# Performance work log

Measured on AMD Instinct MI355X. Metric: run time of the kernel, lower is better.

## Reference

```python
import jax, jax.numpy as jnp
import numpy as np

EPS = 1e-5

def rmsnorm(x):
    # BitLinear pre-norm (no learnable scale), per BitNet b1.58 reference impl
    return x * jax.lax.rsqrt(jnp.mean(x * x, axis=-1, keepdims=True) + EPS)

def act_quant(x):
    # per-token absmax 8-bit quantization with straight-through estimator
    scale = 127.0 / jnp.clip(jnp.max(jnp.abs(x), axis=-1, keepdims=True), 1e-5)
    q = jnp.clip(jnp.round(x * scale), -128.0, 127.0) / scale
    return x + jax.lax.stop_gradient(q - x)

def weight_quant(w):
    # absmean ternary quantization {-1,0,1} with STE
    scale = 1.0 / jnp.clip(jnp.mean(jnp.abs(w)), 1e-5)
    q = jnp.clip(jnp.round(w * scale), -1.0, 1.0) / scale
    return w + jax.lax.stop_gradient(q - w)

def bitlinear(x, w, b):
    # x: [b, s, d_in], w: [d_out, d_in] (torch Linear layout), b: [d_out]
    xq = act_quant(rmsnorm(x))
    wq = weight_quant(w)
    return jnp.einsum('bsd,fd->bsf', xq, wq) + b

def setup_inputs() -> dict:
    key = jax.random.key(0)
    k0, k1, k2 = jax.random.split(key, 3)
    B, S, D, F = 2, 8192, 1024, 4096  # inner_dim = dim * mult = 4096
    x = jax.random.normal(k0, (B, S, D), dtype=jnp.float32)
    w1 = jax.random.normal(k1, (F, D), dtype=jnp.float32) * (1.0 / np.sqrt(D))
    b1 = jnp.zeros((F,), dtype=jnp.float32)
    w2 = jax.random.normal(k2, (D, F), dtype=jnp.float32) * (1.0 / np.sqrt(F))
    b2 = jnp.zeros((D,), dtype=jnp.float32)
    return {"x": x, "w1": w1, "b1": b1, "w2": w2, "b2": b2}

def reference(x, w1, b1, w2, b2):
    h = bitlinear(x, w1, b1)
    h = jax.nn.gelu(h, approximate=False)  # nn.GELU() default is exact
    # post_act_ln=False -> no LayerNorm; dropout p=0.0 -> identity
    return bitlinear(h, w2, b2)
```

## Files before the change

### kernel.cpp

```cpp
#include <hip/hip_runtime.h>
#include <hip/hip_bf16.h>
#include <stdint.h>

typedef int i32x4 __attribute__((ext_vector_type(4)));

__device__ __forceinline__ float blo(unsigned int u) {
  unsigned int v = u << 16; float f; __builtin_memcpy(&f, &v, 4); return f;
}
__device__ __forceinline__ float bhi(unsigned int u) {
  unsigned int v = u & 0xffff0000u; float f; __builtin_memcpy(&f, &v, 4); return f;
}
__device__ __forceinline__ int pack4q(float a, float b, float c, float d, float qm) {
  int i0 = (int)rintf(a * qm) & 255;
  int i1 = (int)rintf(b * qm) & 255;
  int i2 = (int)rintf(c * qm) & 255;
  int i3 = (int)rintf(d * qm) & 255;
  return i0 | (i1 << 8) | (i2 << 16) | (i3 << 24);
}

__device__ __forceinline__ float fast_gelu(float v) {
  float u = v * 0.70710678118654752f;
  float s = fabsf(u);
  float den = fmaf(0.3275911f, s, 1.0f);
  float t;
  asm("v_rcp_f32 %0, %1" : "=v"(t) : "v"(den));
  float p = t * fmaf(t, fmaf(t, fmaf(t, fmaf(t, 1.061405429f, -1.453152027f),
                                     1.421413741f), -0.284496736f), 0.254829592f);
  float e = fmaf(-p, __expf(-u * u), 1.0f);
  float er = copysignf(e, u);
  return 0.5f * v * (1.0f + er);
}

__global__ void k_reduce_abs2(const float* __restrict__ w1, const float* __restrict__ w2,
                              long n4, float* __restrict__ partials) {
  const int half = gridDim.x >> 1;
  const float* w = (blockIdx.x < half) ? w1 : w2;
  int b = (blockIdx.x < half) ? blockIdx.x : blockIdx.x - half;
  const float4* wv = (const float4*)w;
  float s = 0.0f;
  long stride = (long)half * blockDim.x;
  for (long i = (long)b * blockDim.x + threadIdx.x; i < n4; i += stride) {
    float4 v = wv[i];
    s += fabsf(v.x) + fabsf(v.y) + fabsf(v.z) + fabsf(v.w);
  }
  #pragma unroll
  for (int off = 32; off; off >>= 1) s += __shfl_down(s, off);
  __shared__ float sw[4];
  if ((threadIdx.x & 63) == 0) sw[threadIdx.x >> 6] = s;
  __syncthreads();
  if (threadIdx.x == 0) partials[blockIdx.x] = sw[0] + sw[1] + sw[2] + sw[3];
}

__global__ void k_finalize_scales(const float* __restrict__ p1, const float* __restrict__ p2,
                                  float* __restrict__ scales, float inv1, float inv2) {
  int t = threadIdx.x;
  float s1 = p1[t], s2 = p2[t];
  #pragma unroll
  for (int off = 32; off; off >>= 1) { s1 += __shfl_down(s1, off); s2 += __shfl_down(s2, off); }
  __shared__ float a1[4], a2[4];
  if ((t & 63) == 0) { a1[t >> 6] = s1; a2[t >> 6] = s2; }
  __syncthreads();
  if (t == 0) {
    scales[0] = fmaxf((a1[0]+a1[1]+a1[2]+a1[3]) * inv1, 1e-5f);
    scales[1] = fmaxf((a2[0]+a2[1]+a2[2]+a2[3]) * inv2, 1e-5f);
  }
}

__global__ void k_quant_w2(const float* __restrict__ w1, char* __restrict__ wq1,
                           const float* __restrict__ w2, char* __restrict__ wq2,
                           long n4, const float* __restrict__ scales) {
  const int half = gridDim.x >> 1;
  const bool first = blockIdx.x < half;
  const float* w = first ? w1 : w2;
  char* wq = first ? wq1 : wq2;
  int b = first ? blockIdx.x : blockIdx.x - half;
  float s = 1.0f / scales[first ? 0 : 1];
  const float4* wv = (const float4*)w;
  int* qv = (int*)wq;
  long stride = (long)half * blockDim.x;
  for (long i = (long)b * blockDim.x + threadIdx.x; i < n4; i += stride) {
    float4 v = wv[i];
    int b0 = (int)fminf(fmaxf(rintf(v.x * s), -1.0f), 1.0f) & 255;
    int b1 = (int)fminf(fmaxf(rintf(v.y * s), -1.0f), 1.0f) & 255;
    int b2 = (int)fminf(fmaxf(rintf(v.z * s), -1.0f), 1.0f) & 255;
    int b3 = (int)fminf(fmaxf(rintf(v.w * s), -1.0f), 1.0f) & 255;
    qv[i] = b0 | (b1 << 8) | (b2 << 16) | (b3 << 24);
  }
}

__global__ void k_actq_x(const float* __restrict__ x, char* __restrict__ xq,
                         float* __restrict__ alpha) {
  const int D = 1024;
  size_t t = blockIdx.x;
  int tid = threadIdx.x;
  const float4* row = (const float4*)(x + t * (size_t)D);
  float4 v = row[tid];
  float ss = v.x*v.x + v.y*v.y + v.z*v.z + v.w*v.w;
  float am = fmaxf(fmaxf(fabsf(v.x), fabsf(v.y)), fmaxf(fabsf(v.z), fabsf(v.w)));
  #pragma unroll
  for (int off = 32; off; off >>= 1) {
    ss += __shfl_down(ss, off);
    am = fmaxf(am, __shfl_down(am, off));
  }
  __shared__ float s_ss[4], s_am[4];
  if ((tid & 63) == 0) { s_ss[tid >> 6] = ss; s_am[tid >> 6] = am; }
  __syncthreads();
  ss = s_ss[0] + s_ss[1] + s_ss[2] + s_ss[3];
  am = fmaxf(fmaxf(s_am[0], s_am[1]), fmaxf(s_am[2], s_am[3]));
  float rms = rsqrtf(ss * (1.0f / D) + 1e-5f);
  float a   = fmaxf(am * rms, 1e-5f);
  float qs  = 127.0f / a;
  if (tid == 0) alpha[t] = a * (1.0f / 127.0f);
  int b0 = (int)fminf(fmaxf(rintf((v.x * rms) * qs), -128.0f), 127.0f) & 255;
  int b1 = (int)fminf(fmaxf(rintf((v.y * rms) * qs), -128.0f), 127.0f) & 255;
  int b2 = (int)fminf(fmaxf(rintf((v.z * rms) * qs), -128.0f), 127.0f) & 255;
  int b3 = (int)fminf(fmaxf(rintf((v.w * rms) * qs), -128.0f), 127.0f) & 255;
  ((int*)xq)[t * 256 + tid] = b0 | (b1 << 8) | (b2 << 16) | (b3 << 24);
}

__global__ void k_actq_h(__hip_bfloat16* __restrict__ h, float* __restrict__ alpha) {
  const int F = 4096;
  size_t t = blockIdx.x;
  int tid = threadIdx.x;
  char* rb = (char*)(h + t * (size_t)F);
  const uint4* row = (const uint4*)rb;
  uint4 u0 = row[tid], u1 = row[tid + 256];
  unsigned int uu[8] = {u0.x, u0.y, u0.z, u0.w, u1.x, u1.y, u1.z, u1.w};
  float ss = 0.0f, am = 0.0f;
  #pragma unroll
  for (int i = 0; i < 8; i++) {
    float f0 = blo(uu[i]), f1 = bhi(uu[i]);
    ss += f0 * f0 + f1 * f1;
    am = fmaxf(am, fmaxf(fabsf(f0), fabsf(f1)));
  }
  #pragma unroll
  for (int off = 32; off; off >>= 1) {
    ss += __shfl_down(ss, off);
    am = fmaxf(am, __shfl_down(am, off));
  }
  __shared__ float s_ss[4], s_am[4];
  if ((tid & 63) == 0) { s_ss[tid >> 6] = ss; s_am[tid >> 6] = am; }
  __syncthreads();
  ss = s_ss[0] + s_ss[1] + s_ss[2] + s_ss[3];
  am = fmaxf(fmaxf(s_am[0], s_am[1]), fmaxf(s_am[2], s_am[3]));
  float rms = rsqrtf(ss * (1.0f / F) + 1e-5f);
  float a   = fmaxf(am * rms, 1e-5f);
  float qm  = rms * (127.0f / a);
  if (tid == 0) alpha[t] = a * (1.0f / 127.0f);
  uint2 w0, w1;
  w0.x = (unsigned)pack4q(blo(uu[0]), bhi(uu[0]), blo(uu[1]), bhi(uu[1]), qm);
  w0.y = (unsigned)pack4q(blo(uu[2]), bhi(uu[2]), blo(uu[3]), bhi(uu[3]), qm);
  w1.x = (unsigned)pack4q(blo(uu[4]), bhi(uu[4]), blo(uu[5]), bhi(uu[5]), qm);
  w1.y = (unsigned)pack4q(blo(uu[6]), bhi(uu[6]), blo(uu[7]), bhi(uu[7]), qm);
  *(uint2*)(rb + 8 * tid) = w0;
  *(uint2*)(rb + 2048 + 8 * tid) = w1;
}

#define GLD16(GP, LP) __builtin_amdgcn_global_load_lds( \
    (__attribute__((address_space(1))) void*)(GP), \
    (__attribute__((address_space(3))) void*)(LP), 16, 0, 0)
#define VMCNT3 asm volatile("s_waitcnt vmcnt(3)" ::: "memory")
#define VMCNT0 asm volatile("s_waitcnt vmcnt(0)" ::: "memory")
#define LGKM0  do { asm volatile("s_waitcnt lgkmcnt(0)" ::: "memory"); __builtin_amdgcn_sched_barrier(0); } while(0)

template<int EPI>
__global__ __launch_bounds__(512, 4) void k_gemm_i8(
    const char* __restrict__ A, int lda,
    const char* __restrict__ B,
    const float* __restrict__ bias, const float* __restrict__ alpha,
    const float* __restrict__ scales, int which,
    void* __restrict__ Cout, int N, int K, int lgnbx)
{
  __shared__ __align__(16) char lA[3 * 8192];
  __shared__ __align__(16) char lB[3 * 16384];
  const int tid = threadIdx.x, lane = tid & 63, wid = tid >> 6;
  const int wm = wid >> 2, wn = wid & 3;
  const int nwg = gridDim.x, bid = blockIdx.x;
  const int swz = (bid & 7) * (nwg >> 3) + (bid >> 3);
  const int bx = swz & ((1 << lgnbx) - 1), by = swz >> lgnbx;
  const int m0 = by * 128, n0 = bx * 256;
  const int NT = K >> 6;

  const int srow = tid >> 2, slot = tid & 3;
  const int sswz = (slot ^ ((srow >> 1) & 3)) * 16;
  const char* gA0 = A + (size_t)(m0 +       srow) * lda + sswz;
  const char* gB0 = B + (size_t)(n0 +       srow) * K   + sswz;
  const char* gB1 = B + (size_t)(n0 + 128 + srow) * K   + sswz;
  const int ldst = srow * 64 + slot * 16;

  const int lr = lane & 15;
  const int kx = ((lane >> 4) ^ ((lane >> 1) & 3)) * 16;
  const int aoff = (wm * 64 + lr) * 64 + kx;
  const int boff = (wn * 64 + lr) * 64 + kx;

  GLD16(gA0,      lA + ldst);
  GLD16(gB0,      lB + ldst);
  GLD16(gB1,      lB + 8192 + ldst);
  GLD16(gA0 + 64, lA + 8192 + ldst);
  GLD16(gB0 + 64, lB + 16384 + ldst);
  GLD16(gB1 + 64, lB + 16384 + 8192 + ldst);

  i32x4 acc[4][4] = {};
  int cur = 0, nx1 = 1, nx2 = 2;
  for (int t = 0; t < NT; ++t) {
    if (t + 1 < NT) { VMCNT3; } else { VMCNT0; }
    __builtin_amdgcn_s_barrier();
    if (t + 2 < NT) {
      GLD16(gA0 + 64 * (t + 2), lA + nx2 * 8192 + ldst);
      GLD16(gB0 + 64 * (t + 2), lB + nx2 * 16384 + ldst);
      GLD16(gB1 + 64 * (t + 2), lB + nx2 * 16384 + 8192 + ldst);
    }
    i32x4 av[4], bv[4];
    {
      const char* pa = lA + cur * 8192 + aoff;
      const char* pb = lB + cur * 16384 + boff;
      #pragma unroll
      for (int j = 0; j < 4; ++j) av[j] = *(const i32x4*)(pa + j * 1024);
      #pragma unroll
      for (int n = 0; n < 4; ++n) bv[n] = *(const i32x4*)(pb + n * 1024);
    }
    LGKM0;
    __builtin_amdgcn_s_setprio(1);
    #pragma unroll
    for (int j = 0; j < 4; ++j)
      #pragma unroll
      for (int n = 0; n < 4; ++n)
        acc[j][n] = __builtin_amdgcn_mfma_i32_16x16x64_i8(av[j], bv[n], acc[j][n], 0, 0, 0);
    __builtin_amdgcn_s_setprio(0);
    int tmp = cur; cur = nx1; nx1 = nx2; nx2 = tmp;
  }

  const float wdq = scales[which];
  const int lq4 = (lane >> 4) * 4;
  #pragma unroll
  for (int m = 0; m < 4; ++m) {
    const int rowb = m0 + wm * 64 + m * 16 + lq4;
    float al[4];
    #pragma unroll
    for (int q = 0; q < 4; ++q) al[q] = alpha[rowb + q] * wdq;
    #pragma unroll
    for (int n = 0; n < 4; ++n) {
      const int col = n0 + wn * 64 + n * 16 + lr;
      const float bb = bias[col];
      #pragma unroll
      for (int q = 0; q < 4; ++q) {
        float v = (float)acc[m][n][q] * al[q] + bb;
        if constexpr (EPI == 0) {
          ((__hip_bfloat16*)Cout)[(size_t)(rowb + q) * N + col] = __float2bfloat16(fast_gelu(v));
        } else {
          ((float*)Cout)[(size_t)(rowb + q) * N + col] = v;
        }
      }
    }
  }
}

extern "C" void kernel_launch(void* const* d_in, const int* in_sizes, int n_in,
                              void* d_out, int out_size, void* d_ws, size_t ws_size,
                              hipStream_t stream) {
  const float* x  = (const float*)d_in[0];
  const float* w1 = (const float*)d_in[1];
  const float* b1 = (const float*)d_in[2];
  const float* w2 = (const float*)d_in[3];
  const float* b2 = (const float*)d_in[4];
  const int  F = in_sizes[2];
  const int  D = in_sizes[4];
  const long T = (long)in_sizes[0] / D;
  const long nW = (long)F * D;

  char* ws = (char*)d_ws;
  float* partials = (float*)ws;
  float* scales   = partials + 512;
  float* alpha1 = (float*)(ws + 4096);
  float* alpha2 = alpha1 + T;
  size_t off = 4096 + 2 * (size_t)T * sizeof(float);
  off = (off + 255) & ~(size_t)255;
  char* w1q = ws + off; off += (size_t)nW;
  char* w2q = ws + off; off += (size_t)nW;
  char* xq  = ws + off; off += (size_t)T * D;
  off = (off + 255) & ~(size_t)255;
  __hip_bfloat16* h = (__hip_bfloat16*)(ws + off); off += (size_t)T * F * 2;
  if (ws_size < off) return;

  float invW = (float)(1.0 / (double)nW);
  k_reduce_abs2<<<512, 256, 0, stream>>>(w1, w2, nW / 4, partials);
  k_finalize_scales<<<1, 256, 0, stream>>>(partials, partials + 256, scales, invW, invW);
  k_quant_w2<<<4096, 256, 0, stream>>>(w1, w1q, w2, w2q, nW / 4, scales);
  k_actq_x<<<(unsigned)T, 256, 0, stream>>>(x, xq, alpha1);

  dim3 g1((unsigned)((T / 128) * (F / 256)));
  k_gemm_i8<0><<<g1, 512, 0, stream>>>(xq, D, w1q, b1, alpha1, scales, 0,
                                       h, F, D, __builtin_ctz(F / 256));

  k_actq_h<<<(unsigned)T, 256, 0, stream>>>(h, alpha2);

  dim3 g2((unsigned)((T / 128) * (D / 256)));
  k_gemm_i8<1><<<g2, 512, 0, stream>>>((const char*)h, F * 2, w2q, b2, alpha2, scales, 1,
                                       (float*)d_out, D, F, __builtin_ctz(D / 256));
}
```

Before: 244.4 us.

## Load GEMM B operand straight into registers and fold scale finalize into quant

The int8 GEMM no longer stages the weight (B) tile through LDS. Each wave now loads its B fragments directly from global memory into registers, with one-tile-ahead prefetch, while A still uses the triple-buffered LDS pipeline. This is meant to cut LDS traffic and footprint, but B is no longer shared across the two wm waves, so global/L2 load traffic for B doubles, and the loads use a 16-row stride that may coalesce poorly. Separately, the finalize-scales kernel is folded into the weight-quant kernel, where every block re-reduces the partials, saving one launch.

```diff
diff --git a/kernel.cpp b/kernel.cpp
--- a/kernel.cpp
+++ b/kernel.cpp
@@ -51,34 +51,29 @@
   if (threadIdx.x == 0) partials[blockIdx.x] = sw[0] + sw[1] + sw[2] + sw[3];
 }
 
-__global__ void k_finalize_scales(const float* __restrict__ p1, const float* __restrict__ p2,
-                                  float* __restrict__ scales, float inv1, float inv2) {
-  int t = threadIdx.x;
-  float s1 = p1[t], s2 = p2[t];
-  #pragma unroll
-  for (int off = 32; off; off >>= 1) { s1 += __shfl_down(s1, off); s2 += __shfl_down(s2, off); }
-  __shared__ float a1[4], a2[4];
-  if ((t & 63) == 0) { a1[t >> 6] = s1; a2[t >> 6] = s2; }
-  __syncthreads();
-  if (t == 0) {
-    scales[0] = fmaxf((a1[0]+a1[1]+a1[2]+a1[3]) * inv1, 1e-5f);
-    scales[1] = fmaxf((a2[0]+a2[1]+a2[2]+a2[3]) * inv2, 1e-5f);
-  }
-}
-
 __global__ void k_quant_w2(const float* __restrict__ w1, char* __restrict__ wq1,
                            const float* __restrict__ w2, char* __restrict__ wq2,
-                           long n4, const float* __restrict__ scales) {
+                           long n4, const float* __restrict__ partials,
+                           float* __restrict__ scales, float invW) {
   const int half = gridDim.x >> 1;
   const bool first = blockIdx.x < half;
+  int t = threadIdx.x;
+  float p = partials[(first ? 0 : 256) + t];
+  #pragma unroll
+  for (int off = 32; off; off >>= 1) p += __shfl_down(p, off);
+  __shared__ float a[4];
+  if ((t & 63) == 0) a[t >> 6] = p;
+  __syncthreads();
+  float sc = fmaxf((a[0] + a[1] + a[2] + a[3]) * invW, 1e-5f);
+  if (t == 0 && (blockIdx.x == 0 || blockIdx.x == half)) scales[first ? 0 : 1] = sc;
+  float s = 1.0f / sc;
   const float* w = first ? w1 : w2;
   char* wq = first ? wq1 : wq2;
   int b = first ? blockIdx.x : blockIdx.x - half;
-  float s = 1.0f / scales[first ? 0 : 1];
   const float4* wv = (const float4*)w;
   int* qv = (int*)wq;
   long stride = (long)half * blockDim.x;
-  for (long i = (long)b * blockDim.x + threadIdx.x; i < n4; i += stride) {
+  for (long i = (long)b * blockDim.x + t; i < n4; i += stride) {
     float4 v = wv[i];
     int b0 = (int)fminf(fmaxf(rintf(v.x * s), -1.0f), 1.0f) & 255;
     int b1 = (int)fminf(fmaxf(rintf(v.y * s), -1.0f), 1.0f) & 255;
@@ -159,12 +154,12 @@
 #define GLD16(GP, LP) __builtin_amdgcn_global_load_lds( \
     (__attribute__((address_space(1))) void*)(GP), \
     (__attribute__((address_space(3))) void*)(LP), 16, 0, 0)
-#define VMCNT3 asm volatile("s_waitcnt vmcnt(3)" ::: "memory")
+#define VMCNT1 asm volatile("s_waitcnt vmcnt(1)" ::: "memory")
 #define VMCNT0 asm volatile("s_waitcnt vmcnt(0)" ::: "memory")
 #define LGKM0  do { asm volatile("s_waitcnt lgkmcnt(0)" ::: "memory"); __builtin_amdgcn_sched_barrier(0); } while(0)
 
 template<int EPI>
-__global__ __launch_bounds__(512, 4) void k_gemm_i8(
+__global__ __launch_bounds__(512, 4) void k_gemm_flat(
     const char* __restrict__ A, int lda,
     const char* __restrict__ B,
     const float* __restrict__ bias, const float* __restrict__ alpha,
@@ -172,7 +167,6 @@
     void* __restrict__ Cout, int N, int K, int lgnbx)
 {
   __shared__ __align__(16) char lA[3 * 8192];
-  __shared__ __align__(16) char lB[3 * 16384];
   const int tid = threadIdx.x, lane = tid & 63, wid = tid >> 6;
   const int wm = wid >> 2, wn = wid & 3;
   const int nwg = gridDim.x, bid = blockIdx.x;
@@ -183,49 +177,46 @@
 
   const int srow = tid >> 2, slot = tid & 3;
   const int sswz = (slot ^ ((srow >> 1) & 3)) * 16;
-  const char* gA0 = A + (size_t)(m0 +       srow) * lda + sswz;
-  const char* gB0 = B + (size_t)(n0 +       srow) * K   + sswz;
-  const char* gB1 = B + (size_t)(n0 + 128 + srow) * K   + sswz;
+  const char* gA = A + (size_t)(m0 + srow) * lda + sswz;
   const int ldst = srow * 64 + slot * 16;
 
   const int lr = lane & 15;
   const int kx = ((lane >> 4) ^ ((lane >> 1) & 3)) * 16;
   const int aoff = (wm * 64 + lr) * 64 + kx;
-  const int boff = (wn * 64 + lr) * 64 + kx;
-
-  GLD16(gA0,      lA + ldst);
-  GLD16(gB0,      lB + ldst);
-  GLD16(gB1,      lB + 8192 + ldst);
-  GLD16(gA0 + 64, lA + 8192 + ldst);
-  GLD16(gB0 + 64, lB + 16384 + ldst);
-  GLD16(gB1 + 64, lB + 16384 + 8192 + ldst);
+
+  const char* gB = B + (size_t)(n0 + wn * 64 + lr) * K + (lane >> 4) * 16;
+  const size_t bstep = (size_t)16 * K;
+
+  i32x4 bcur[4], bnext[4];
+  #pragma unroll
+  for (int n = 0; n < 4; ++n) bnext[n] = *(const i32x4*)(gB + (size_t)n * bstep);
+  GLD16(gA,      lA + ldst);
+  GLD16(gA + 64, lA + 8192 + ldst);
 
   i32x4 acc[4][4] = {};
   int cur = 0, nx1 = 1, nx2 = 2;
   for (int t = 0; t < NT; ++t) {
-    if (t + 1 < NT) { VMCNT3; } else { VMCNT0; }
+    if (t + 1 < NT) { VMCNT1; } else { VMCNT0; }
+    #pragma unroll
+    for (int n = 0; n < 4; ++n) bcur[n] = bnext[n];
     __builtin_amdgcn_s_barrier();
-    if (t + 2 < NT) {
-      GLD16(gA0 + 64 * (t + 2), lA + nx2 * 8192 + ldst);
-      GLD16(gB0 + 64 * (t + 2), lB + nx2 * 16384 + ldst);
-      GLD16(gB1 + 64 * (t + 2), lB + nx2 * 16384 + 8192 + ldst);
+    if (t + 1 < NT) {
+      const char* gb = gB + (size_t)(t + 1) * 64;
+      #pragma unroll
+      for (int n = 0; n < 4; ++n) bnext[n] = *(const i32x4*)(gb + (size_t)n * bstep);
     }
-    i32x4 av[4], bv[4];
-    {
-      const char* pa = lA + cur * 8192 + aoff;
-      const char* pb = lB + cur * 16384 + boff;
-      #pragma unroll
-      for (int j = 0; j < 4; ++j) av[j] = *(const i32x4*)(pa + j * 1024);
-      #pragma unroll
-      for (int n = 0; n < 4; ++n) bv[n] = *(const i32x4*)(pb + n * 1024);
-    }
+    if (t + 2 < NT) GLD16(gA + 64 * (t + 2), lA + nx2 * 8192 + ldst);
+    const char* pa = lA + cur * 8192 + aoff;
+    i32x4 av[4];
+    #pragma unroll
+    for (int j = 0; j < 4; ++j) av[j] = *(const i32x4*)(pa + j * 1024);
     LGKM0;
     __builtin_amdgcn_s_setprio(1);
     #pragma unroll
     for (int j = 0; j < 4; ++j)
       #pragma unroll
       for (int n = 0; n < 4; ++n)
-        acc[j][n] = __builtin_amdgcn_mfma_i32_16x16x64_i8(av[j], bv[n], acc[j][n], 0, 0, 0);
+        acc[j][n] = __builtin_amdgcn_mfma_i32_16x16x64_i8(av[j], bcur[n], acc[j][n], 0, 0, 0);
     __builtin_amdgcn_s_setprio(0);
     int tmp = cur; cur = nx1; nx1 = nx2; nx2 = tmp;
   }
@@ -284,17 +275,16 @@
 
   float invW = (float)(1.0 / (double)nW);
   k_reduce_abs2<<<512, 256, 0, stream>>>(w1, w2, nW / 4, partials);
-  k_finalize_scales<<<1, 256, 0, stream>>>(partials, partials + 256, scales, invW, invW);
-  k_quant_w2<<<4096, 256, 0, stream>>>(w1, w1q, w2, w2q, nW / 4, scales);
+  k_quant_w2<<<4096, 256, 0, stream>>>(w1, w1q, w2, w2q, nW / 4, partials, scales, invW);
   k_actq_x<<<(unsigned)T, 256, 0, stream>>>(x, xq, alpha1);
 
   dim3 g1((unsigned)((T / 128) * (F / 256)));
-  k_gemm_i8<0><<<g1, 512, 0, stream>>>(xq, D, w1q, b1, alpha1, scales, 0,
-                                       h, F, D, __builtin_ctz(F / 256));
+  k_gemm_flat<0><<<g1, 512, 0, stream>>>(xq, D, w1q, b1, alpha1, scales, 0,
+                                         h, F, D, __builtin_ctz(F / 256));
 
   k_actq_h<<<(unsigned)T, 256, 0, stream>>>(h, alpha2);
 
   dim3 g2((unsigned)((T / 128) * (D / 256)));
-  k_gemm_i8<1><<<g2, 512, 0, stream>>>((const char*)h, F * 2, w2q, b2, alpha2, scales, 1,
-                                       (float*)d_out, D, F, __builtin_ctz(D / 256));
-}
+  k_gemm_flat<1><<<g2, 512, 0, stream>>>((const char*)h, F * 2, w2q, b2, alpha2, scales, 1,
+                                         (float*)d_out, D, F, __builtin_ctz(D / 256));
+}
```

Result: slower. 371.1 us (+51.9%).
